# Kernel optimization log

Hardware: AMD Instinct MI355X
Metric: run time of the kernel (lower is better)

## Reference

```python
import jax, jax.numpy as jnp
import numpy as np

N = 32768      # num nodes
F = 128        # raw node feature dim
D = 128        # embedding_dim
E = 524288     # num edges (avg degree 16)
L = 8          # transformer depth
H = 8          # heads
CS = 32        # target_cluster_size
NC = 10        # num classes
K = N // CS    # num clusters (all full -> pad branch is a no-op)


def _leaky_relu(x):
    return jnp.where(x >= 0, x, 0.2 * x)


def _gat(h_in, src, dst, W, a_src, a_dst, b):
    # PyG GATConv, heads=1, with self-loops already appended to src/dst
    h = h_in @ W                                             # [N, D]
    e = _leaky_relu((h @ a_src)[src] + (h @ a_dst)[dst])     # [E+N]
    m = jax.ops.segment_max(e, dst, num_segments=N)
    ex = jnp.exp(e - m[dst])
    denom = jax.ops.segment_sum(ex, dst, num_segments=N)
    alpha = ex / denom[dst]
    return jax.ops.segment_sum(h[src] * alpha[:, None], dst, num_segments=N) + b


def _ln(x, s, b):
    m = x.mean(-1, keepdims=True)
    v = ((x - m) ** 2).mean(-1, keepdims=True)
    return (x - m) * jax.lax.rsqrt(v + 1e-5) * s + b


def setup_inputs() -> dict:
    key = jax.random.key(0)
    ks = jax.random.split(key, 20)
    rn = lambda k, s, sc=0.05: jax.random.normal(k, s, jnp.float32) * sc
    return dict(
        x=jax.random.normal(ks[0], (N, F), jnp.float32),
        edge_index=jax.random.randint(ks[1], (2, E), 0, N),
        node_order=jax.random.permutation(ks[2], N).astype(jnp.int32),
        W_in=rn(ks[3], (F, D)), b_in=jnp.zeros(D, jnp.float32),
        Wg1=rn(ks[4], (D, D)), as1=rn(ks[5], (D,)), ad1=rn(ks[6], (D,)), bg1=jnp.zeros(D, jnp.float32),
        Wg2=rn(ks[7], (D, D)), as2=rn(ks[8], (D,)), ad2=rn(ks[9], (D,)), bg2=jnp.zeros(D, jnp.float32),
        W_emb=rn(ks[10], (CS * D, D), 0.02), b_emb=jnp.zeros(D, jnp.float32),
        cls_tok=rn(ks[11], (D,)),
        ln1_s=jnp.ones((L, D), jnp.float32), ln1_b=jnp.zeros((L, D), jnp.float32),
        Wqkv=rn(ks[12], (L, D, 3 * D)), bqkv=jnp.zeros((L, 3 * D), jnp.float32),
        Wo=rn(ks[13], (L, D, D)), bo=jnp.zeros((L, D), jnp.float32),
        ln2_s=jnp.ones((L, D), jnp.float32), ln2_b=jnp.zeros((L, D), jnp.float32),
        Wf1=rn(ks[14], (L, D, 4 * D)), bf1=jnp.zeros((L, 4 * D), jnp.float32),
        Wf2=rn(ks[15], (L, 4 * D, D)), bf2=jnp.zeros((L, D), jnp.float32),
        Wc=rn(ks[16], (D, NC)), bc=jnp.zeros(NC, jnp.float32),
    )


def reference(x, edge_index, node_order, W_in, b_in, Wg1, as1, ad1, bg1,
              Wg2, as2, ad2, bg2, W_emb, b_emb, cls_tok,
              ln1_s, ln1_b, Wqkv, bqkv, Wo, bo, ln2_s, ln2_b,
              Wf1, bf1, Wf2, bf2, Wc, bc):
    loops = jnp.arange(N, dtype=edge_index.dtype)
    src = jnp.concatenate([edge_index[0], loops])
    dst = jnp.concatenate([edge_index[1], loops])
    h = x @ W_in + b_in
    h = _gat(h, src, dst, Wg1, as1, ad1, bg1)
    h = _gat(h, src, dst, Wg2, as2, ad2, bg2)
    # irregular cluster gather, then per-cluster linear embedding (32*D -> D)
    flat = h[node_order].reshape(K, CS * D)
    emb = flat @ W_emb + b_emb                               # [K, D]
    t = jnp.concatenate([cls_tok[None, :], emb], axis=0)     # [K+1, D]
    dh = D // H
    scale = dh ** -0.5
    for l in range(L):                                       # pre-norm transformer
        u = _ln(t, ln1_s[l], ln1_b[l])
        qkv = u @ Wqkv[l] + bqkv[l]
        q, k, v = [a.reshape(-1, H, dh) for a in jnp.split(qkv, 3, axis=-1)]
        att = jax.nn.softmax(jnp.einsum('qhd,khd->hqk', q, k) * scale, axis=-1)
        o = jnp.einsum('hqk,khd->qhd', att, v).reshape(-1, D) @ Wo[l] + bo[l]
        t = t + o
        u = _ln(t, ln2_s[l], ln2_b[l])
        t = t + jax.nn.gelu(u @ Wf1[l] + bf1[l]) @ Wf2[l] + bf2[l]
    return (t[0] @ Wc + bc)[None, :]                         # [1, NC]
```

## Files before the change

kernel.cpp:

```cpp
#include <hip/hip_runtime.h>
#include <hip/hip_bf16.h>
#include <math.h>

#define NN 32768
#define NE 524288
#define EN_TOT (NE + NN)
#define LL 8
#define SS 1025
#define SPLIT 16

__global__ void hist_kernel(const int* __restrict__ ei, int* __restrict__ cnt) {
    int i = blockIdx.x * 256 + threadIdx.x;
    if (i >= EN_TOT) return;
    int d = (i < NE) ? ei[NE + i] : (i - NE);
    atomicAdd(&cnt[d], 1);
}

__global__ void scan_kernel(const int* __restrict__ cnt, int* __restrict__ offs) {
    __shared__ int wsum[16];
    int t = threadIdx.x;
    int base = t * 32;
    int s = 0;
    #pragma unroll
    for (int j = 0; j < 32; ++j) s += cnt[base + j];
    int lane = t & 63, w = t >> 6;
    int v = s;
    #pragma unroll
    for (int d = 1; d < 64; d <<= 1) {
        int u = __shfl_up(v, d);
        if (lane >= d) v += u;
    }
    if (lane == 63) wsum[w] = v;
    __syncthreads();
    if (t == 0) {
        int a = 0;
        #pragma unroll
        for (int i = 0; i < 16; ++i) { int x = wsum[i]; wsum[i] = a; a += x; }
    }
    __syncthreads();
    int run = wsum[w] + (v - s);
    #pragma unroll
    for (int j = 0; j < 32; ++j) { offs[base + j] = run; run += cnt[base + j]; }
    if (t == 1023) offs[NN] = run;
}

__global__ void scatter_kernel(const int* __restrict__ ei, const int* __restrict__ offs,
                               int* __restrict__ fill, int* __restrict__ csr) {
    int i = blockIdx.x * 256 + threadIdx.x;
    if (i >= EN_TOT) return;
    int s, d;
    if (i < NE) { s = ei[i]; d = ei[NE + i]; } else { s = d = i - NE; }
    int pos = offs[d] + atomicAdd(&fill[d], 1);
    csr[pos] = s;
}

__device__ __forceinline__ float gelu_f(float x) {
    float x3 = x * x * x;
    return 0.5f * x * (1.f + tanhf(0.7978845608028654f * (x + 0.044715f * x3)));
}

__global__ void gemm_f32(const float* __restrict__ A, const float* __restrict__ B,
                         const float* __restrict__ bias, const float* res,
                         float* C, __hip_bfloat16* Cb,
                         const float* __restrict__ asv, const float* __restrict__ adv,
                         float* ssv, float* sdv,
                         int M, int Nn, int K) {
    __shared__ float As[32][66];
    __shared__ float Bs[32][72];
    int t = threadIdx.x;
    int bx = blockIdx.x, by = blockIdx.y;
    int tx = t & 15, ty = t >> 4;
    float acc[4][4] = {};
    int m0 = t >> 3;
    int kk4 = (t & 7) * 4;
    int kb0 = t >> 4;
    int n40 = (t & 15) * 4;

    for (int k0 = 0; k0 < K; k0 += 32) {
        __syncthreads();
        #pragma unroll
        for (int half = 0; half < 2; ++half) {
            int m = m0 + half * 32;
            int row = by * 64 + m;
            float4 v = {0.f, 0.f, 0.f, 0.f};
            if (row < M) v = *(const float4*)&A[(size_t)row * K + k0 + kk4];
            As[kk4 + 0][m] = v.x; As[kk4 + 1][m] = v.y;
            As[kk4 + 2][m] = v.z; As[kk4 + 3][m] = v.w;
        }
        #pragma unroll
        for (int half = 0; half < 2; ++half) {
            int kk = kb0 + half * 16;
            *(float4*)&Bs[kk][n40] = *(const float4*)&B[(size_t)(k0 + kk) * Nn + bx * 64 + n40];
        }
        __syncthreads();
        #pragma unroll
        for (int kk = 0; kk < 32; ++kk) {
            float a0 = As[kk][ty * 4 + 0];
            float a1 = As[kk][ty * 4 + 1];
            float a2 = As[kk][ty * 4 + 2];
            float a3 = As[kk][ty * 4 + 3];
            float4 b4 = *(float4*)&Bs[kk][tx * 4];
            acc[0][0] += a0 * b4.x; acc[0][1] += a0 * b4.y; acc[0][2] += a0 * b4.z; acc[0][3] += a0 * b4.w;
            acc[1][0] += a1 * b4.x; acc[1][1] += a1 * b4.y; acc[1][2] += a1 * b4.z; acc[1][3] += a1 * b4.w;
            acc[2][0] += a2 * b4.x; acc[2][1] += a2 * b4.y; acc[2][2] += a2 * b4.z; acc[2][3] += a2 * b4.w;
            acc[3][0] += a3 * b4.x; acc[3][1] += a3 * b4.y; acc[3][2] += a3 * b4.z; acc[3][3] += a3 * b4.w;
        }
    }
    #pragma unroll
    for (int i = 0; i < 4; ++i) {
        int row = by * 64 + ty * 4 + i;
        if (row < M) {
            #pragma unroll
            for (int j = 0; j < 4; ++j) {
                int col = bx * 64 + tx * 4 + j;
                float v = acc[i][j];
                if (bias) v += bias[col];
                if (res) v += res[(size_t)row * Nn + col];
                acc[i][j] = v;
                C[(size_t)row * Nn + col] = v;
                if (Cb) Cb[(size_t)row * Nn + col] = __float2bfloat16(v);
            }
        }
    }
    if (asv) {
        #pragma unroll
        for (int i = 0; i < 4; ++i) {
            int row = by * 64 + ty * 4 + i;
            float vs = 0.f, vd = 0.f;
            #pragma unroll
            for (int j = 0; j < 4; ++j) {
                int col = bx * 64 + tx * 4 + j;
                vs += acc[i][j] * asv[col];
                vd += acc[i][j] * adv[col];
            }
            #pragma unroll
            for (int m = 8; m >= 1; m >>= 1) { vs += __shfl_xor(vs, m); vd += __shfl_xor(vd, m); }
            if (tx == 0 && row < M) {
                atomicAdd(&ssv[row], vs);
                atomicAdd(&sdv[row], vd);
            }
        }
    }
}

__global__ void bcomb_kernel(const float* __restrict__ b_in, const float* __restrict__ Wg1,
                             float* __restrict__ bcomb) {
    int n = threadIdx.x;
    float s = 0.f;
    for (int k = 0; k < 128; ++k) s += b_in[k] * Wg1[k * 128 + n];
    bcomb[n] = s;
}

__global__ void emb_gemm(const float* __restrict__ h, const float* __restrict__ W,
                         const int* __restrict__ no, float* __restrict__ pbuf) {
    __shared__ float As[32][66];
    __shared__ float Bs[32][72];
    int t = threadIdx.x;
    int bx = blockIdx.x, by = blockIdx.y, sp = blockIdx.z;
    int tx = t & 15, ty = t >> 4;
    float acc[4][4] = {};
    int m0 = t >> 3;
    int kk4 = (t & 7) * 4;
    int kb0 = t >> 4;
    int n40 = (t & 15) * 4;
    int kbase = sp * 256;

    for (int k0 = 0; k0 < 256; k0 += 32) {
        __syncthreads();
        #pragma unroll
        for (int half = 0; half < 2; ++half) {
            int m = m0 + half * 32;
            int row = by * 64 + m;
            int kg = kbase + k0 + kk4;
            int node = no[row * 32 + (kg >> 7)];
            float4 v = *(const float4*)&h[(size_t)node * 128 + (kg & 127)];
            As[kk4 + 0][m] = v.x; As[kk4 + 1][m] = v.y;
            As[kk4 + 2][m] = v.z; As[kk4 + 3][m] = v.w;
        }
        #pragma unroll
        for (int half = 0; half < 2; ++half) {
            int kk = kb0 + half * 16;
            *(float4*)&Bs[kk][n40] = *(const float4*)&W[(size_t)(kbase + k0 + kk) * 128 + bx * 64 + n40];
        }
        __syncthreads();
        #pragma unroll
        for (int kk = 0; kk < 32; ++kk) {
            float a0 = As[kk][ty * 4 + 0];
            float a1 = As[kk][ty * 4 + 1];
            float a2 = As[kk][ty * 4 + 2];
            float a3 = As[kk][ty * 4 + 3];
            float4 b4 = *(float4*)&Bs[kk][tx * 4];
            acc[0][0] += a0 * b4.x; acc[0][1] += a0 * b4.y; acc[0][2] += a0 * b4.z; acc[0][3] += a0 * b4.w;
            acc[1][0] += a1 * b4.x; acc[1][1] += a1 * b4.y; acc[1][2] += a1 * b4.z; acc[1][3] += a1 * b4.w;
            acc[2][0] += a2 * b4.x; acc[2][1] += a2 * b4.y; acc[2][2] += a2 * b4.z; acc[2][3] += a2 * b4.w;
            acc[3][0] += a3 * b4.x; acc[3][1] += a3 * b4.y; acc[3][2] += a3 * b4.z; acc[3][3] += a3 * b4.w;
        }
    }
    float* C = pbuf + (size_t)sp * (1024 * 128);
    #pragma unroll
    for (int i = 0; i < 4; ++i) {
        int row = by * 64 + ty * 4 + i;
        #pragma unroll
        for (int j = 0; j < 4; ++j)
            C[(size_t)row * 128 + bx * 64 + tx * 4 + j] = acc[i][j];
    }
}

__global__ void emb_reduce(const float* __restrict__ pbuf, const float* __restrict__ b_emb,
                           float* __restrict__ out) {
    int i = blockIdx.x * 256 + threadIdx.x;
    float s = b_emb[i & 127];
    #pragma unroll
    for (int sp = 0; sp < SPLIT; ++sp) s += pbuf[(size_t)sp * 131072 + i];
    out[i] = s;
}

__global__ void gat_aggregate(const unsigned* __restrict__ hWb, const int* __restrict__ offs,
                              const int* __restrict__ csr, const float* __restrict__ ssrc,
                              const float* __restrict__ sdst, const float* __restrict__ bias,
                              float* __restrict__ out) {
    int lane = threadIdx.x & 63;
    int n = blockIdx.x * 4 + (threadIdx.x >> 6);
    int beg = offs[n], end = offs[n + 1];
    float sd = sdst[n];
    float mymax = -INFINITY;
    for (int p = beg + lane; p < end; p += 64) {
        float e = ssrc[csr[p]] + sd;
        e = (e >= 0.f) ? e : 0.2f * e;
        mymax = fmaxf(mymax, e);
    }
    #pragma unroll
    for (int m = 32; m >= 1; m >>= 1) mymax = fmaxf(mymax, __shfl_xor(mymax, m));
    float mysum = 0.f;
    for (int p = beg + lane; p < end; p += 64) {
        float e = ssrc[csr[p]] + sd;
        e = (e >= 0.f) ? e : 0.2f * e;
        mysum += __expf(e - mymax);
    }
    #pragma unroll
    for (int m = 32; m >= 1; m >>= 1) mysum += __shfl_xor(mysum, m);
    float inv = 1.f / mysum;
    float acc0 = 0.f, acc1 = 0.f;
    for (int p = beg; p < end; ++p) {
        int s = csr[p];
        float e = ssrc[s] + sd;
        e = (e >= 0.f) ? e : 0.2f * e;
        float al = __expf(e - mymax) * inv;
        unsigned u = hWb[(size_t)s * 64 + lane];
        float f0 = __uint_as_float(u << 16);
        float f1 = __uint_as_float(u & 0xffff0000u);
        acc0 += al * f0;
        acc1 += al * f1;
    }
    float2 ov;
    ov.x = acc0 + bias[2 * lane];
    ov.y = acc1 + bias[2 * lane + 1];
    *(float2*)&out[(size_t)n * 128 + 2 * lane] = ov;
}

__global__ __launch_bounds__(256) void qkv_slice(
        const float* __restrict__ tb, const float* __restrict__ s1, const float* __restrict__ b1,
        const float* __restrict__ Wq, const float* __restrict__ bq, float* __restrict__ qkv) {
    __shared__ float u[4][128];
    __shared__ float red[4][2][128];
    __shared__ float ws[8192];
    int t = threadIdx.x;
    int r0 = blockIdx.x * 4, sl = blockIdx.y;
    int col = t & 127, kh = t >> 7;
    {
        int rw = t >> 6, lane = t & 63;
        int row = r0 + rw;
        float a0 = 0.f, a1 = 0.f;
        if (row < SS) {
            a0 = tb[(size_t)row * 128 + lane];
            a1 = tb[(size_t)row * 128 + 64 + lane];
        }
        float sm = a0 + a1;
        #pragma unroll
        for (int m = 32; m >= 1; m >>= 1) sm += __shfl_xor(sm, m);
        float mean = sm * (1.f / 128.f);
        float d0 = a0 - mean, d1 = a1 - mean;
        float vv = d0 * d0 + d1 * d1;
        #pragma unroll
        for (int m = 32; m >= 1; m >>= 1) vv += __shfl_xor(vv, m);
        float rs = rsqrtf(vv * (1.f / 128.f) + 1e-5f);
        u[rw][lane] = d0 * rs * s1[lane] + b1[lane];
        u[rw][64 + lane] = d1 * rs * s1[64 + lane] + b1[64 + lane];
    }
    float acc[4] = {};
    for (int k0 = 0; k0 < 128; k0 += 64) {
        __syncthreads();
        const float* src = Wq + (size_t)k0 * 384 + sl * 128;
        #pragma unroll
        for (int i = 0; i < 8; ++i) {
            int idx = i * 256 + t;
            int kk = idx >> 5, c4 = (idx & 31) * 4;
            ((float4*)ws)[idx] = *(const float4*)&src[(size_t)kk * 384 + c4];
        }
        __syncthreads();
        int kb = kh * 32;
        #pragma unroll
        for (int kq = 0; kq < 32; kq += 4) {
            float a4[4][4];
            #pragma unroll
            for (int i = 0; i < 4; ++i)
                *(float4*)a4[i] = *(const float4*)&u[i][k0 + kb + kq];
            #pragma unroll
            for (int q = 0; q < 4; ++q) {
                float b = ws[(kb + kq + q) * 128 + col];
                #pragma unroll
                for (int i = 0; i < 4; ++i) acc[i] += a4[i][q] * b;
            }
        }
    }
    __syncthreads();
    #pragma unroll
    for (int i = 0; i < 4; ++i) red[i][kh][col] = acc[i];
    __syncthreads();
    if (t < 128) {
        float bqv = bq[sl * 128 + t];
        #pragma unroll
        for (int i = 0; i < 4; ++i) {
            int row = r0 + i;
            if (row < SS)
                qkv[(size_t)row * 384 + sl * 128 + t] = red[i][0][t] + red[i][1][t] + bqv;
        }
    }
}

__global__ __launch_bounds__(256) void proj_ln2(
        const float* __restrict__ ao, const float* __restrict__ Wo, const float* __restrict__ bo,
        const float* __restrict__ s2, const float* __restrict__ b2, const float* __restrict__ bf2,
        float* __restrict__ tb, float* __restrict__ ub) {
    __shared__ float bufA[4][128];
    __shared__ float tn[4][128];
    __shared__ float red[4][2][128];
    __shared__ float ws[8192];
    int t = threadIdx.x;
    int r0 = blockIdx.x * 4;
    int lane = t & 63;
    int col = t & 127, kh = t >> 7;
    {
        int rw = t >> 6;
        int row = r0 + rw;
        float a0 = 0.f, a1 = 0.f;
        if (row < SS) {
            a0 = ao[(size_t)row * 128 + lane];
            a1 = ao[(size_t)row * 128 + 64 + lane];
        }
        bufA[rw][lane] = a0;
        bufA[rw][64 + lane] = a1;
    }
    float pp[4] = {};
    for (int k0 = 0; k0 < 128; k0 += 64) {
        __syncthreads();
        const float4* src = (const float4*)&Wo[(size_t)k0 * 128];
        #pragma unroll
        for (int i = 0; i < 8; ++i) ((float4*)ws)[i * 256 + t] = src[i * 256 + t];
        __syncthreads();
        int kb = kh * 32;
        #pragma unroll
        for (int kq = 0; kq < 32; kq += 4) {
            float a4[4][4];
            #pragma unroll
            for (int i = 0; i < 4; ++i)
                *(float4*)a4[i] = *(const float4*)&bufA[i][k0 + kb + kq];
            #pragma unroll
            for (int q = 0; q < 4; ++q) {
                float b = ws[(kb + kq + q) * 128 + col];
                #pragma unroll
                for (int i = 0; i < 4; ++i) pp[i] += a4[i][q] * b;
            }
        }
    }
    __syncthreads();
    #pragma unroll
    for (int i = 0; i < 4; ++i) red[i][kh][col] = pp[i];
    __syncthreads();
    if (t < 128) {
        #pragma unroll
        for (int i = 0; i < 4; ++i) {
            int row = r0 + i;
            float v = 0.f;
            if (row < SS) {
                v = red[i][0][t] + red[i][1][t] + bo[t] + tb[(size_t)row * 128 + t];
                tb[(size_t)row * 128 + t] = v + bf2[t];
            }
            tn[i][t] = v;
        }
    }
    __syncthreads();
    {
        int rw = t >> 6;
        int row = r0 + rw;
        float a0 = tn[rw][lane], a1 = tn[rw][64 + lane];
        float sm = a0 + a1;
        #pragma unroll
        for (int m = 32; m >= 1; m >>= 1) sm += __shfl_xor(sm, m);
        float mean = sm * (1.f / 128.f);
        float d0 = a0 - mean, d1 = a1 - mean;
        float vv = d0 * d0 + d1 * d1;
        #pragma unroll
        for (int m = 32; m >= 1; m >>= 1) vv += __shfl_xor(vv, m);
        float rs = rsqrtf(vv * (1.f / 128.f) + 1e-5f);
        if (row < SS) {
            ub[(size_t)row * 128 + lane] = d0 * rs * s2[lane] + b2[lane];
            ub[(size_t)row * 128 + 64 + lane] = d1 * rs * s2[64 + lane] + b2[64 + lane];
        }
    }
}

__global__ __launch_bounds__(256) void ffn_part(
        const float* __restrict__ ub, const float* __restrict__ Wf1, const float* __restrict__ bf1,
        const float* __restrict__ Wf2, float* __restrict__ tb) {
    __shared__ float u[4][128];
    __shared__ float g[4][128];
    __shared__ float red[4][2][128];
    __shared__ float ws[8192];
    int t = threadIdx.x;
    int r0 = blockIdx.x * 4, sl = blockIdx.y;
    int col = t & 127, kh = t >> 7;
    {
        int rw = t >> 6, lane = t & 63;
        int row = r0 + rw;
        float a0 = 0.f, a1 = 0.f;
        if (row < SS) {
            a0 = ub[(size_t)row * 128 + lane];
            a1 = ub[(size_t)row * 128 + 64 + lane];
        }
        u[rw][lane] = a0;
        u[rw][64 + lane] = a1;
    }
    float a1c[4] = {};
    for (int k0 = 0; k0 < 128; k0 += 64) {
        __syncthreads();
        const float* src = Wf1 + (size_t)k0 * 512 + sl * 128;
        #pragma unroll
        for (int i = 0; i < 8; ++i) {
            int idx = i * 256 + t;
            int kk = idx >> 5, c4 = (idx & 31) * 4;
            ((float4*)ws)[idx] = *(const float4*)&src[(size_t)kk * 512 + c4];
        }
        __syncthreads();
        int kb = kh * 32;
        #pragma unroll
        for (int kq = 0; kq < 32; kq += 4) {
            float a4[4][4];
            #pragma unroll
            for (int i = 0; i < 4; ++i)
                *(float4*)a4[i] = *(const float4*)&u[i][k0 + kb + kq];
            #pragma unroll
            for (int q = 0; q < 4; ++q) {
                float b = ws[(kb + kq + q) * 128 + col];
                #pragma unroll
                for (int i = 0; i < 4; ++i) a1c[i] += a4[i][q] * b;
            }
        }
    }
    __syncthreads();
    #pragma unroll
    for (int i = 0; i < 4; ++i) red[i][kh][col] = a1c[i];
    __syncthreads();
    if (t < 128) {
        float bv = bf1[sl * 128 + t];
        #pragma unroll
        for (int i = 0; i < 4; ++i)
            g[i][t] = gelu_f(red[i][0][t] + red[i][1][t] + bv);
    }
    float a2c[4] = {};
    for (int k0 = 0; k0 < 128; k0 += 64) {
        __syncthreads();
        const float4* src = (const float4*)&Wf2[(size_t)(sl * 128 + k0) * 128];
        #pragma unroll
        for (int i = 0; i < 8; ++i) ((float4*)ws)[i * 256 + t] = src[i * 256 + t];
        __syncthreads();
        int kb = kh * 32;
        #pragma unroll
        for (int kq = 0; kq < 32; kq += 4) {
            float a4[4][4];
            #pragma unroll
            for (int i = 0; i < 4; ++i)
                *(float4*)a4[i] = *(const float4*)&g[i][k0 + kb + kq];
            #pragma unroll
            for (int q = 0; q < 4; ++q) {
                float b = ws[(kb + kq + q) * 128 + col];
                #pragma unroll
                for (int i = 0; i < 4; ++i) a2c[i] += a4[i][q] * b;
            }
        }
    }
    __syncthreads();
    #pragma unroll
    for (int i = 0; i < 4; ++i) red[i][kh][col] = a2c[i];
    __syncthreads();
    if (t < 128) {
        #pragma unroll
        for (int i = 0; i < 4; ++i) {
            int row = r0 + i;
            if (row < SS)
                atomicAdd(&tb[(size_t)row * 128 + t], red[i][0][t] + red[i][1][t]);
        }
    }
}

__global__ void attn_kernel(const float* __restrict__ qkv, float* __restrict__ ao) {
    __shared__ float Kl[64][20];
    __shared__ float Vl[64][20];
    int h = blockIdx.y;
    int t = threadIdx.x;
    int sub = t & 15;
    int qr = blockIdx.x * 16 + (t >> 4);
    bool active = qr < SS;
    float q[16];
    if (active) {
        #pragma unroll
        for (int d = 0; d < 16; ++d) q[d] = qkv[(size_t)qr * 384 + h * 16 + d];
    }
    float m = -INFINITY, sum = 0.f;
    float acc[16] = {};
    for (int j0 = 0; j0 < SS; j0 += 64) {
        __syncthreads();
        int j = t >> 2, dg = (t & 3) * 4;
        if (j0 + j < SS) {
            const float* row = qkv + (size_t)(j0 + j) * 384 + h * 16 + dg;
            *(float4*)&Kl[j][dg] = *(const float4*)(row + 128);
            *(float4*)&Vl[j][dg] = *(const float4*)(row + 256);
        }
        __syncthreads();
        if (active) {
            int jmax = min(64, SS - j0);
            for (int jj = sub; jj < jmax; jj += 16) {
                float4 ka = *(const float4*)&Kl[jj][0];
                float4 kb = *(const float4*)&Kl[jj][4];
                float4 kc = *(const float4*)&Kl[jj][8];
                float4 kd = *(const float4*)&Kl[jj][12];
                float sc = q[0]*ka.x + q[1]*ka.y + q[2]*ka.z + q[3]*ka.w
                         + q[4]*kb.x + q[5]*kb.y + q[6]*kb.z + q[7]*kb.w
                         + q[8]*kc.x + q[9]*kc.y + q[10]*kc.z + q[11]*kc.w
                         + q[12]*kd.x + q[13]*kd.y + q[14]*kd.z + q[15]*kd.w;
                sc *= 0.25f;
                float4 va = *(const float4*)&Vl[jj][0];
                float4 vb = *(const float4*)&Vl[jj][4];
                float4 vc = *(const float4*)&Vl[jj][8];
                float4 vd = *(const float4*)&Vl[jj][12];
                float vv[16] = {va.x, va.y, va.z, va.w, vb.x, vb.y, vb.z, vb.w,
                                vc.x, vc.y, vc.z, vc.w, vd.x, vd.y, vd.z, vd.w};
                if (sc <= m) {
                    float p = __expf(sc - m);
                    sum += p;
                    #pragma unroll
                    for (int d = 0; d < 16; ++d) acc[d] += p * vv[d];
                } else {
                    float c = __expf(m - sc);
                    sum = sum * c + 1.f;
                    #pragma unroll
                    for (int d = 0; d < 16; ++d) acc[d] = acc[d] * c + vv[d];
                    m = sc;
                }
            }
        }
    }
    if (active) {
        #pragma unroll
        for (int msk = 1; msk < 16; msk <<= 1) {
            float mo = __shfl_xor(m, msk);
            float so = __shfl_xor(sum, msk);
            float vo[16];
            #pragma unroll
            for (int d = 0; d < 16; ++d) vo[d] = __shfl_xor(acc[d], msk);
            float mn = fmaxf(m, mo);
            float c1 = __expf(m - mn), c2 = __expf(mo - mn);
            sum = sum * c1 + so * c2;
            #pragma unroll
            for (int d = 0; d < 16; ++d) acc[d] = acc[d] * c1 + vo[d] * c2;
            m = mn;
        }
        if (sub == 0) {
            float inv = 1.f / sum;
            #pragma unroll
            for (int d = 0; d < 16; ++d) ao[(size_t)qr * 128 + h * 16 + d] = acc[d] * inv;
        }
    }
}

__global__ void cls_copy(const float* __restrict__ c, float* __restrict__ t) {
    t[threadIdx.x] = c[threadIdx.x];
}

__global__ void classifier_kernel(const float* __restrict__ t, const float* __restrict__ Wc,
                                  const float* __restrict__ bc, float* __restrict__ out) {
    int j = threadIdx.x;
    if (j < 10) {
        float a = bc[j];
        #pragma unroll
        for (int k = 0; k < 128; ++k) a += t[k] * Wc[k * 10 + j];
        out[j] = a;
    }
}

extern "C" void kernel_launch(void* const* d_in, const int* in_sizes, int n_in,
                              void* d_out, int out_size, void* d_ws, size_t ws_size,
                              hipStream_t stream) {
    (void)in_sizes; (void)n_in; (void)out_size; (void)ws_size;
    const float* x     = (const float*)d_in[0];
    const int*   ei    = (const int*)d_in[1];
    const int*   nord  = (const int*)d_in[2];
    const float* W_in  = (const float*)d_in[3];
    const float* b_in  = (const float*)d_in[4];
    const float* Wg1   = (const float*)d_in[5];
    const float* as1   = (const float*)d_in[6];
    const float* ad1   = (const float*)d_in[7];
    const float* bg1   = (const float*)d_in[8];
    const float* Wg2   = (const float*)d_in[9];
    const float* as2   = (const float*)d_in[10];
    const float* ad2   = (const float*)d_in[11];
    const float* bg2   = (const float*)d_in[12];
    const float* W_emb = (const float*)d_in[13];
    const float* b_emb = (const float*)d_in[14];
    const float* clst  = (const float*)d_in[15];
    const float* ln1s  = (const float*)d_in[16];
    const float* ln1b  = (const float*)d_in[17];
    const float* Wqkv  = (const float*)d_in[18];
    const float* bqkv  = (const float*)d_in[19];
    const float* Wo    = (const float*)d_in[20];
    const float* bo    = (const float*)d_in[21];
    const float* ln2s  = (const float*)d_in[22];
    const float* ln2b  = (const float*)d_in[23];
    const float* Wf1   = (const float*)d_in[24];
    const float* bf1   = (const float*)d_in[25];
    const float* Wf2   = (const float*)d_in[26];
    const float* bf2   = (const float*)d_in[27];
    const float* Wc    = (const float*)d_in[28];
    const float* bc    = (const float*)d_in[29];

    char* w = (char*)d_ws;
    size_t o = 0;
    auto ALLOC = [&](size_t nbytes) -> char* {
        char* p = w + o;
        o += (nbytes + 255) & ~(size_t)255;
        return p;
    };
    int*   cnt   = (int*)ALLOC((size_t)NN * 4);
    int*   fill  = (int*)ALLOC((size_t)NN * 4);
    int*   offs  = (int*)ALLOC((size_t)(NN + 1) * 4);
    int*   csr   = (int*)ALLOC((size_t)EN_TOT * 4);
    float* hA    = (float*)ALLOC((size_t)NN * 128 * 4);
    float* hW    = (float*)ALLOC((size_t)NN * 128 * 4);
    float* h1    = (float*)ALLOC((size_t)NN * 128 * 4);
    __hip_bfloat16* hWb = (__hip_bfloat16*)ALLOC((size_t)NN * 128 * 2);
    float* ssrc  = (float*)ALLOC((size_t)NN * 4);
    float* sdst  = (float*)ALLOC((size_t)NN * 4);
    float* tbuf  = (float*)ALLOC((size_t)SS * 128 * 4);
    float* ubuf  = (float*)ALLOC((size_t)SS * 128 * 4);
    float* qkvb  = (float*)ALLOC((size_t)SS * 384 * 4);
    float* aob   = (float*)ALLOC((size_t)SS * 128 * 4);
    float* Wcomb = (float*)ALLOC((size_t)128 * 128 * 4);
    float* bcomb = (float*)ALLOC((size_t)128 * 4);
    float* pbuf  = hW;

    dim3 blk(256);
    int egrid = (EN_TOT + 255) / 256;

    hipMemsetAsync(cnt, 0, (size_t)NN * 8, stream);
    hist_kernel<<<egrid, blk, 0, stream>>>(ei, cnt);
    scan_kernel<<<1, 1024, 0, stream>>>(cnt, offs);
    scatter_kernel<<<egrid, blk, 0, stream>>>(ei, offs, fill, csr);

    gemm_f32<<<dim3(2, 2), blk, 0, stream>>>(W_in, Wg1, nullptr, nullptr, Wcomb,
                                             nullptr, nullptr, nullptr, nullptr, nullptr,
                                             128, 128, 128);
    bcomb_kernel<<<1, 128, 0, stream>>>(b_in, Wg1, bcomb);

    hipMemsetAsync(ssrc, 0, (size_t)NN * 8, stream);
    gemm_f32<<<dim3(2, 512), blk, 0, stream>>>(x, Wcomb, bcomb, nullptr, hW,
                                               hWb, as1, ad1, ssrc, sdst,
                                               NN, 128, 128);
    gat_aggregate<<<8192, blk, 0, stream>>>((const unsigned*)hWb, offs, csr, ssrc, sdst, bg1, h1);
    hipMemsetAsync(ssrc, 0, (size_t)NN * 8, stream);
    gemm_f32<<<dim3(2, 512), blk, 0, stream>>>(h1, Wg2, nullptr, nullptr, hW,
                                               hWb, as2, ad2, ssrc, sdst,
                                               NN, 128, 128);
    gat_aggregate<<<8192, blk, 0, stream>>>((const unsigned*)hWb, offs, csr, ssrc, sdst, bg2, hA);

    cls_copy<<<1, 128, 0, stream>>>(clst, tbuf);
    emb_gemm<<<dim3(2, 16, SPLIT), blk, 0, stream>>>(hA, W_emb, nord, pbuf);
    emb_reduce<<<512, blk, 0, stream>>>(pbuf, b_emb, tbuf + 128);

    for (int l = 0; l < LL; ++l) {
        qkv_slice<<<dim3(257, 3), blk, 0, stream>>>(tbuf, ln1s + l * 128, ln1b + l * 128,
                                                    Wqkv + (size_t)l * 128 * 384, bqkv + l * 384, qkvb);
        attn_kernel<<<dim3(65, 8), blk, 0, stream>>>(qkvb, aob);
        proj_ln2<<<257, blk, 0, stream>>>(aob, Wo + (size_t)l * 128 * 128, bo + l * 128,
                                          ln2s + l * 128, ln2b + l * 128, bf2 + l * 128,
                                          tbuf, ubuf);
        ffn_part<<<dim3(257, 4), blk, 0, stream>>>(ubuf, Wf1 + (size_t)l * 128 * 512, bf1 + l * 512,
                                                   Wf2 + (size_t)l * 512 * 128, tbuf);
    }
    classifier_kernel<<<1, 64, 0, stream>>>(tbuf, Wc, bc, (float*)d_out);
}
```

Before: 874.2 us.

## Aggregate GAT in fp32 with edge-parallel shuffles and pre-gather cluster embedding input

The GEMM no longer writes a bf16 copy of the projected features, and GAT aggregation reads fp32 rows directly. Each wave now loads neighbor indices and attention weights in parallel, broadcasts them with shuffles, and has two half-waves process different edges using float4 row loads. The cluster gather for the embedding GEMM moves into a separate gather_copy kernel that writes a contiguous flat buffer, so the GEMM's A loads become coalesced. The cost is twice the gather bandwidth per neighbor row in the aggregation, plus an extra kernel pass over 16 MB for the flat buffer.

```diff
diff --git a/kernel.cpp b/kernel.cpp
--- a/kernel.cpp
+++ b/kernel.cpp
@@ -61,7 +61,7 @@
 
 __global__ void gemm_f32(const float* __restrict__ A, const float* __restrict__ B,
                          const float* __restrict__ bias, const float* res,
-                         float* C, __hip_bfloat16* Cb,
+                         float* C,
                          const float* __restrict__ asv, const float* __restrict__ adv,
                          float* ssv, float* sdv,
                          int M, int Nn, int K) {
@@ -118,7 +118,6 @@
                 if (res) v += res[(size_t)row * Nn + col];
                 acc[i][j] = v;
                 C[(size_t)row * Nn + col] = v;
-                if (Cb) Cb[(size_t)row * Nn + col] = __float2bfloat16(v);
             }
         }
     }
@@ -151,8 +150,16 @@
     bcomb[n] = s;
 }
 
-__global__ void emb_gemm(const float* __restrict__ h, const float* __restrict__ W,
-                         const int* __restrict__ no, float* __restrict__ pbuf) {
+__global__ void gather_copy(const float* __restrict__ hA, const int* __restrict__ no,
+                            float* __restrict__ flat) {
+    int i = blockIdx.x * 256 + threadIdx.x;
+    int m = i >> 12, j = i & 4095;
+    int node = no[(m << 5) + (j >> 7)];
+    flat[i] = hA[(size_t)node * 128 + (j & 127)];
+}
+
+__global__ void emb_gemm(const float* __restrict__ flat, const float* __restrict__ W,
+                         float* __restrict__ pbuf) {
     __shared__ float As[32][66];
     __shared__ float Bs[32][72];
     int t = threadIdx.x;
@@ -171,9 +178,7 @@
         for (int half = 0; half < 2; ++half) {
             int m = m0 + half * 32;
             int row = by * 64 + m;
-            int kg = kbase + k0 + kk4;
-            int node = no[row * 32 + (kg >> 7)];
-            float4 v = *(const float4*)&h[(size_t)node * 128 + (kg & 127)];
+            float4 v = *(const float4*)&flat[(size_t)row * 4096 + kbase + k0 + kk4];
             As[kk4 + 0][m] = v.x; As[kk4 + 1][m] = v.y;
             As[kk4 + 2][m] = v.z; As[kk4 + 3][m] = v.w;
         }
@@ -215,47 +220,78 @@
     out[i] = s;
 }
 
-__global__ void gat_aggregate(const unsigned* __restrict__ hWb, const int* __restrict__ offs,
+__global__ void gat_aggregate(const float* __restrict__ hW, const int* __restrict__ offs,
                               const int* __restrict__ csr, const float* __restrict__ ssrc,
                               const float* __restrict__ sdst, const float* __restrict__ bias,
                               float* __restrict__ out) {
     int lane = threadIdx.x & 63;
     int n = blockIdx.x * 4 + (threadIdx.x >> 6);
-    int beg = offs[n], end = offs[n + 1];
+    int beg = offs[n], deg = offs[n + 1] - beg;
     float sd = sdst[n];
     float mymax = -INFINITY;
-    for (int p = beg + lane; p < end; p += 64) {
-        float e = ssrc[csr[p]] + sd;
-        e = (e >= 0.f) ? e : 0.2f * e;
-        mymax = fmaxf(mymax, e);
+    for (int c0 = 0; c0 < deg; c0 += 64) {
+        if (c0 + lane < deg) {
+            int s = csr[beg + c0 + lane];
+            float e = ssrc[s] + sd;
+            e = (e >= 0.f) ? e : 0.2f * e;
+            mymax = fmaxf(mymax, e);
+        }
     }
     #pragma unroll
     for (int m = 32; m >= 1; m >>= 1) mymax = fmaxf(mymax, __shfl_xor(mymax, m));
     float mysum = 0.f;
-    for (int p = beg + lane; p < end; p += 64) {
-        float e = ssrc[csr[p]] + sd;
-        e = (e >= 0.f) ? e : 0.2f * e;
-        mysum += __expf(e - mymax);
+    for (int c0 = 0; c0 < deg; c0 += 64) {
+        if (c0 + lane < deg) {
+            int s = csr[beg + c0 + lane];
+            float e = ssrc[s] + sd;
+            e = (e >= 0.f) ? e : 0.2f * e;
+            mysum += __expf(e - mymax);
+        }
     }
     #pragma unroll
     for (int m = 32; m >= 1; m >>= 1) mysum += __shfl_xor(mysum, m);
     float inv = 1.f / mysum;
-    float acc0 = 0.f, acc1 = 0.f;
-    for (int p = beg; p < end; ++p) {
-        int s = csr[p];
-        float e = ssrc[s] + sd;
-        e = (e >= 0.f) ? e : 0.2f * e;
-        float al = __expf(e - mymax) * inv;
-        unsigned u = hWb[(size_t)s * 64 + lane];
-        float f0 = __uint_as_float(u << 16);
-        float f1 = __uint_as_float(u & 0xffff0000u);
-        acc0 += al * f0;
-        acc1 += al * f1;
-    }
-    float2 ov;
-    ov.x = acc0 + bias[2 * lane];
-    ov.y = acc1 + bias[2 * lane + 1];
-    *(float2*)&out[(size_t)n * 128 + 2 * lane] = ov;
+    float ax = 0.f, ay = 0.f, az = 0.f, aw = 0.f;
+    int half = lane >> 5, col = lane & 31;
+    for (int c0 = 0; c0 < deg; c0 += 64) {
+        int s = 0; float al = 0.f;
+        if (c0 + lane < deg) {
+            s = csr[beg + c0 + lane];
+            float e = ssrc[s] + sd;
+            e = (e >= 0.f) ? e : 0.2f * e;
+            al = __expf(e - mymax) * inv;
+        }
+        int cend = min(64, deg - c0);
+        int j = half;
+        for (; j + 2 < cend; j += 4) {
+            int sj0 = __shfl(s, j);
+            float aj0 = __shfl(al, j);
+            int sj1 = __shfl(s, j + 2);
+            float aj1 = __shfl(al, j + 2);
+            float4 v0 = *(const float4*)&hW[(size_t)sj0 * 128 + col * 4];
+            float4 v1 = *(const float4*)&hW[(size_t)sj1 * 128 + col * 4];
+            ax += aj0 * v0.x; ay += aj0 * v0.y; az += aj0 * v0.z; aw += aj0 * v0.w;
+            ax += aj1 * v1.x; ay += aj1 * v1.y; az += aj1 * v1.z; aw += aj1 * v1.w;
+        }
+        for (; j < cend; j += 2) {
+            int sj = __shfl(s, j);
+            float aj = __shfl(al, j);
+            float4 v = *(const float4*)&hW[(size_t)sj * 128 + col * 4];
+            ax += aj * v.x; ay += aj * v.y; az += aj * v.z; aw += aj * v.w;
+        }
+    }
+    ax += __shfl_xor(ax, 32);
+    ay += __shfl_xor(ay, 32);
+    az += __shfl_xor(az, 32);
+    aw += __shfl_xor(aw, 32);
+    if (half == 0) {
+        float4 ov;
+        ov.x = ax + bias[col * 4 + 0];
+        ov.y = ay + bias[col * 4 + 1];
+        ov.z = az + bias[col * 4 + 2];
+        ov.w = aw + bias[col * 4 + 3];
+        *(float4*)&out[(size_t)n * 128 + col * 4] = ov;
+    }
 }
 
 __global__ __launch_bounds__(256) void qkv_slice(
@@ -647,7 +683,6 @@
     float* hA    = (float*)ALLOC((size_t)NN * 128 * 4);
     float* hW    = (float*)ALLOC((size_t)NN * 128 * 4);
     float* h1    = (float*)ALLOC((size_t)NN * 128 * 4);
-    __hip_bfloat16* hWb = (__hip_bfloat16*)ALLOC((size_t)NN * 128 * 2);
     float* ssrc  = (float*)ALLOC((size_t)NN * 4);
     float* sdst  = (float*)ALLOC((size_t)NN * 4);
     float* tbuf  = (float*)ALLOC((size_t)SS * 128 * 4);
@@ -657,6 +692,7 @@
     float* Wcomb = (float*)ALLOC((size_t)128 * 128 * 4);
     float* bcomb = (float*)ALLOC((size_t)128 * 4);
     float* pbuf  = hW;
+    float* flat  = h1;
 
     dim3 blk(256);
     int egrid = (EN_TOT + 255) / 256;
@@ -667,23 +703,24 @@
     scatter_kernel<<<egrid, blk, 0, stream>>>(ei, offs, fill, csr);
 
     gemm_f32<<<dim3(2, 2), blk, 0, stream>>>(W_in, Wg1, nullptr, nullptr, Wcomb,
-                                             nullptr, nullptr, nullptr, nullptr, nullptr,
+                                             nullptr, nullptr, nullptr, nullptr,
                                              128, 128, 128);
     bcomb_kernel<<<1, 128, 0, stream>>>(b_in, Wg1, bcomb);
 
     hipMemsetAsync(ssrc, 0, (size_t)NN * 8, stream);
     gemm_f32<<<dim3(2, 512), blk, 0, stream>>>(x, Wcomb, bcomb, nullptr, hW,
-                                               hWb, as1, ad1, ssrc, sdst,
+                                               as1, ad1, ssrc, sdst,
                                                NN, 128, 128);
-    gat_aggregate<<<8192, blk, 0, stream>>>((const unsigned*)hWb, offs, csr, ssrc, sdst, bg1, h1);
+    gat_aggregate<<<8192, blk, 0, stream>>>(hW, offs, csr, ssrc, sdst, bg1, h1);
     hipMemsetAsync(ssrc, 0, (size_t)NN * 8, stream);
     gemm_f32<<<dim3(2, 512), blk, 0, stream>>>(h1, Wg2, nullptr, nullptr, hW,
-                                               hWb, as2, ad2, ssrc, sdst,
+                                               as2, ad2, ssrc, sdst,
                                                NN, 128, 128);
-    gat_aggregate<<<8192, blk, 0, stream>>>((const unsigned*)hWb, offs, csr, ssrc, sdst, bg2, hA);
+    gat_aggregate<<<8192, blk, 0, stream>>>(hW, offs, csr, ssrc, sdst, bg2, hA);
 
     cls_copy<<<1, 128, 0, stream>>>(clst, tbuf);
-    emb_gemm<<<dim3(2, 16, SPLIT), blk, 0, stream>>>(hA, W_emb, nord, pbuf);
+    gather_copy<<<16384, blk, 0, stream>>>(hA, nord, flat);
+    emb_gemm<<<dim3(2, 16, SPLIT), blk, 0, stream>>>(flat, W_emb, pbuf);
     emb_reduce<<<512, blk, 0, stream>>>(pbuf, b_emb, tbuf + 128);
 
     for (int l = 0; l < LL; ++l) {
```

After: 835.0 us. -4.5%, faster.
